# Kernel tuning notes

Hardware: AMD Instinct MI355X
Metric: run time of the kernel (lower is better)

Reference implementation:

```python
import jax, jax.numpy as jnp
import numpy as np

EPS = 1e-8


def setup_inputs() -> dict:
    key = jax.random.key(0)
    ks = jax.random.split(key, 8)
    B, N, D = 8, 1024, 256
    x = jax.random.normal(ks[0], (B, N, D), dtype=jnp.float32)
    y = jax.random.normal(ks[1], (B, N, D), dtype=jnp.float32)
    coords = jax.random.normal(ks[2], (N, N, 6), dtype=jnp.float32)
    # xavier-ish init for U, kaiming-ish for S1/S2
    U = jax.random.normal(ks[3], (D, D), dtype=jnp.float32) * (1.0 / np.sqrt(D))
    S1 = jax.random.normal(ks[4], (D, 1), dtype=jnp.float32)
    S2 = jax.random.normal(ks[5], (D, 1), dtype=jnp.float32)
    gating = jnp.asarray(1.0, dtype=jnp.float32)
    h_temp = jnp.asarray(0.1, dtype=jnp.float32)
    p_temp = jnp.asarray(1.0, dtype=jnp.float32)
    # trunc_normal_(a=0, b=1): std-normal truncated to [0, 1]
    pos_emb = jax.random.truncated_normal(ks[6], 0.0, 1.0, (N, 6, 1)).astype(jnp.float32)
    return {"x": x, "y": y, "coords": coords, "U": U, "S1": S1, "S2": S2,
            "gating": gating, "h_temp": h_temp, "p_temp": p_temp, "pos_emb": pos_emb}


def _spectral(x, U, S):
    # x @ U.T @ diag(|S|) @ U  ==  ((x @ U.T) * |S|) @ U
    s = jnp.abs(S[:, 0])
    return ((x @ U.T) * s) @ U


def reference(x, y, coords, U, S1, S2, gating, h_temp, p_temp, pos_emb):
    B, N, D = x.shape
    scale = D ** (-0.5)
    xs = jnp.stack([_spectral(x, U, S1), _spectral(x, U, S2)], axis=1)  # [B,2,N,D]
    # patch attention scores: [B,2,N,N]
    patch_score = jax.nn.softmax(jnp.einsum('bknd,bmd->bknm', xs, y) * scale, axis=-1)
    # positional scores, shared across batch and the 2 spectral branches: [N,N]
    pos_logits = -jnp.abs(p_temp) * jnp.einsum('nmc,ncq->nm', coords, pos_emb)
    pos_score = jax.nn.softmax(pos_logits, axis=-1)
    g = jax.nn.sigmoid(gating)
    attn = (1.0 - g) * patch_score + g * pos_score[None, None]  # [B,2,N,N]
    # entropy over key axis -> [B,N,2]
    entropy = jnp.sum(-attn * jnp.log(attn + EPS), axis=-1).transpose(0, 2, 1)
    hmap = 2.0 - 2.0 * jax.nn.sigmoid(h_temp * entropy)  # [B,N,2]
    fgbg = hmap[..., 0] >= hmap[..., 1]
    route = jax.lax.stop_gradient(
        jnp.stack([fgbg, ~fgbg], axis=-1).astype(hmap.dtype))  # [B,N,2]
    heat_map = jnp.sum(hmap * route, axis=-1, keepdims=True)  # [B,N,1]
    attn_sel = jnp.sum(attn * route.transpose(0, 2, 1)[..., None], axis=1)  # [B,N,N]
    out = attn_sel @ y  # [B,N,D]
    return (out, heat_map)
```

## Files before the change

kernel.cpp:

```cpp
#include <hip/hip_runtime.h>
#include <hip/hip_bf16.h>
#include <stdint.h>


#define NB 8
#define NN_ 1024
#define ND 256

typedef __bf16 bf16x8 __attribute__((ext_vector_type(8)));
typedef __bf16 bf16x4 __attribute__((ext_vector_type(4)));
typedef float f32x4 __attribute__((ext_vector_type(4)));

__device__ inline void gl_lds(const __bf16* g, __bf16* l) {
    auto gp = (const __attribute__((address_space(1))) uint32_t*)(uintptr_t)g;
    auto lp = (__attribute__((address_space(3))) uint32_t*)(uintptr_t)l;
    __builtin_amdgcn_global_load_lds(gp, lp, 16, 0, 0);
}

__device__ inline float wred_sum(float v) {
#pragma unroll
    for (int o = 32; o; o >>= 1) v += __shfl_xor(v, o, 64);
    return v;
}
__device__ inline float wred_max(float v) {
#pragma unroll
    for (int o = 32; o; o >>= 1) v = fmaxf(v, __shfl_xor(v, o, 64));
    return v;
}

__global__ __launch_bounds__(256) void prep_kernel(
    const float* __restrict__ coords, const float* __restrict__ pos_emb,
    const float* __restrict__ p_temp, const float* __restrict__ x,
    const float* __restrict__ y, const float* __restrict__ U,
    const float* __restrict__ S1, const float* __restrict__ S2,
    float* __restrict__ posS, __bf16* __restrict__ Xh, __bf16* __restrict__ Xl,
    __bf16* __restrict__ yt, __bf16* __restrict__ Yh, __bf16* __restrict__ Yl,
    __bf16* __restrict__ Mh, __bf16* __restrict__ Ml) {
    __shared__ char sm[9216 + 64];
    const int bid = blockIdx.x;
    const int tid = threadIdx.x;

    if (bid < 1024) {
        float* red = (float*)sm;
        const int n = bid;
        const float pt = -fabsf(p_temp[0]);
        float pe[6];
#pragma unroll
        for (int c = 0; c < 6; ++c) pe[c] = pos_emb[n * 6 + c];
        const float* cr = coords + (long)n * NN_ * 6;
        float l[4];
#pragma unroll
        for (int j = 0; j < 4; ++j) {
            const int m = j * 256 + tid;
            const float2* cp = (const float2*)(cr + (long)m * 6);
            float2 c0 = cp[0], c1 = cp[1], c2 = cp[2];
            l[j] = pt * (c0.x * pe[0] + c0.y * pe[1] + c1.x * pe[2] +
                         c1.y * pe[3] + c2.x * pe[4] + c2.y * pe[5]);
        }
        float mx = fmaxf(fmaxf(l[0], l[1]), fmaxf(l[2], l[3]));
        mx = wred_max(mx);
        __syncthreads();
        if ((tid & 63) == 0) red[tid >> 6] = mx;
        __syncthreads();
        mx = fmaxf(fmaxf(red[0], red[1]), fmaxf(red[2], red[3]));
        float e[4], s = 0.f;
#pragma unroll
        for (int j = 0; j < 4; ++j) { e[j] = __expf(l[j] - mx); s += e[j]; }
        s = wred_sum(s);
        __syncthreads();
        if ((tid & 63) == 0) red[4 + (tid >> 6)] = s;
        __syncthreads();
        s = red[4] + red[5] + red[6] + red[7];
        const float inv = 1.f / s;
#pragma unroll
        for (int j = 0; j < 4; ++j)
            posS[(long)n * NN_ + j * 256 + tid] = e[j] * inv;
    } else if (bid < 1536) {
        const int n4 = NB * NN_ * ND / 4;
        int i = (bid - 1024) * 256 + tid;
        for (; i < n4; i += 512 * 256) {
            float4 v = ((const float4*)x)[i];
            bf16x4 h, l;
            h[0] = (__bf16)v.x; l[0] = (__bf16)(v.x - (float)h[0]);
            h[1] = (__bf16)v.y; l[1] = (__bf16)(v.y - (float)h[1]);
            h[2] = (__bf16)v.z; l[2] = (__bf16)(v.z - (float)h[2]);
            h[3] = (__bf16)v.w; l[3] = (__bf16)(v.w - (float)h[3]);
            ((bf16x4*)Xh)[i] = h;
            ((bf16x4*)Xl)[i] = l;
        }
    } else if (bid < 2048) {
        __bf16 (*t)[72] = (__bf16(*)[72])sm;
        const int rem = bid - 1536;
        const int b = rem >> 6;
        const int m0 = (rem & 15) * 64, d0 = ((rem >> 4) & 3) * 64;
        const int c = tid & 15;
        const int r = tid >> 4;
#pragma unroll
        for (int p = 0; p < 4; ++p) {
            const int row = r + p * 16;
            const long gi = ((long)b * NN_ + m0 + row) * ND + d0 + c * 4;
            float4 v = *(const float4*)(y + gi);
            bf16x4 h, l;
            h[0] = (__bf16)v.x; l[0] = (__bf16)(v.x - (float)h[0]);
            h[1] = (__bf16)v.y; l[1] = (__bf16)(v.y - (float)h[1]);
            h[2] = (__bf16)v.z; l[2] = (__bf16)(v.z - (float)h[2]);
            h[3] = (__bf16)v.w; l[3] = (__bf16)(v.w - (float)h[3]);
            *(bf16x4*)(Yh + gi) = h;
            *(bf16x4*)(Yl + gi) = l;
            t[c * 4 + 0][row] = h[0]; t[c * 4 + 1][row] = h[1];
            t[c * 4 + 2][row] = h[2]; t[c * 4 + 3][row] = h[3];
        }
        __syncthreads();
#pragma unroll
        for (int p = 0; p < 4; ++p) {
            const int d = r + p * 16;
            bf16x4 o;
            o[0] = t[d][c * 4 + 0]; o[1] = t[d][c * 4 + 1];
            o[2] = t[d][c * 4 + 2]; o[3] = t[d][c * 4 + 3];
            *(bf16x4*)(yt + ((long)b * ND + d0 + d) * NN_ + m0 + c * 4) = o;
        }
    } else {
        const int n = bid - 2048, j = tid;
        float a1 = 0.f, a2 = 0.f;
        for (int c = 0; c < ND; ++c) {
            const float un = U[c * ND + n];
            const float uj = U[c * ND + j];
            a1 = fmaf(fabsf(S1[c]) * un, uj, a1);
            a2 = fmaf(fabsf(S2[c]) * un, uj, a2);
        }
        const __bf16 h1 = (__bf16)a1, h2 = (__bf16)a2;
        Mh[n * ND + j] = h1;           Ml[n * ND + j] = (__bf16)(a1 - (float)h1);
        Mh[65536 + n * ND + j] = h2;   Ml[65536 + n * ND + j] = (__bf16)(a2 - (float)h2);
    }
}

__global__ __launch_bounds__(256) void mgemm_xs(
    const __bf16* __restrict__ Ah, const __bf16* __restrict__ Al,
    const __bf16* __restrict__ Bh, const __bf16* __restrict__ Bl,
    __bf16* __restrict__ Ch, __bf16* __restrict__ Cl,
    int M, int N, int K, long sB1, long sC) {
    constexpr int BM = 64, BK = 32, BN = 64;
    __shared__ __bf16 As[2][2 * BM * BK];
    __shared__ __bf16 Bs[2][2 * BN * BK];

    const int z = blockIdx.z;
    Bh += (long)z * sB1; Bl += (long)z * sB1;

    const int tid = threadIdx.x;
    const int bm = blockIdx.y * BM, bn = blockIdx.x * BN;
    const int wave = tid >> 6, lane = tid & 63;
    const int wm = wave >> 1, wn = wave & 1;
    const int quad = lane >> 4, l16 = lane & 15;
    const int srow = lane >> 2, slot = lane & 3;

    f32x4 acc[2][2];
#pragma unroll
    for (int i = 0; i < 2; ++i)
#pragma unroll
        for (int j = 0; j < 2; ++j) acc[i][j] = (f32x4){0.f, 0.f, 0.f, 0.f};

    auto stage = [&](int sel, int k0) {
        const int r0 = wave * 16;
        const int row = r0 + srow;
        const int chunk = slot ^ ((row >> 1) & 3);
        const long ga = (long)(bm + row) * K + k0 + chunk * 8;
        gl_lds(Ah + ga, &As[sel][r0 * 32]);
        gl_lds(Al + ga, &As[sel][BM * BK + r0 * 32]);
        const long gb = (long)(bn + row) * K + k0 + chunk * 8;
        gl_lds(Bh + gb, &Bs[sel][r0 * 32]);
        gl_lds(Bl + gb, &Bs[sel][BN * BK + r0 * 32]);
    };

    stage(0, 0);
    __syncthreads();
    int cur = 0;
    for (int k0 = 0; k0 < K; k0 += BK) {
        if (k0 + BK < K) stage(cur ^ 1, k0 + BK);

        bf16x8 a_h[2], a_l[2], b_h[2], b_l[2];
#pragma unroll
        for (int mi = 0; mi < 2; ++mi) {
            const int row = wm * 32 + mi * 16 + l16;
            const int off = row * 32 + ((quad ^ ((row >> 1) & 3)) * 8);
            a_h[mi] = *(const bf16x8*)&As[cur][off];
            a_l[mi] = *(const bf16x8*)&As[cur][BM * BK + off];
        }
#pragma unroll
        for (int ni = 0; ni < 2; ++ni) {
            const int row = wn * 32 + ni * 16 + l16;
            const int off = row * 32 + ((quad ^ ((row >> 1) & 3)) * 8);
            b_h[ni] = *(const bf16x8*)&Bs[cur][off];
            b_l[ni] = *(const bf16x8*)&Bs[cur][BN * BK + off];
        }
#pragma unroll
        for (int mi = 0; mi < 2; ++mi)
#pragma unroll
            for (int ni = 0; ni < 2; ++ni) {
                acc[mi][ni] = __builtin_amdgcn_mfma_f32_16x16x32_bf16(
                    a_h[mi], b_h[ni], acc[mi][ni], 0, 0, 0);
                acc[mi][ni] = __builtin_amdgcn_mfma_f32_16x16x32_bf16(
                    a_h[mi], b_l[ni], acc[mi][ni], 0, 0, 0);
                acc[mi][ni] = __builtin_amdgcn_mfma_f32_16x16x32_bf16(
                    a_l[mi], b_h[ni], acc[mi][ni], 0, 0, 0);
            }

        __syncthreads();
        cur ^= 1;
    }

    Ch += (long)z * sC; Cl += (long)z * sC;
#pragma unroll
    for (int mi = 0; mi < 2; ++mi) {
        const int row0 = bm + wm * 32 + mi * 16 + quad * 4;
#pragma unroll
        for (int ni = 0; ni < 2; ++ni) {
            const int col = bn + wn * 32 + ni * 16 + l16;
#pragma unroll
            for (int r = 0; r < 4; ++r) {
                const float v = acc[mi][ni][r];
                const long idx = (long)(row0 + r) * N + col;
                const __bf16 h = (__bf16)v;
                Ch[idx] = h;
                Cl[idx] = (__bf16)(v - (float)h);
            }
        }
    }
}

__global__ __launch_bounds__(256) void mgemm_sc(
    const __bf16* __restrict__ Ah, const __bf16* __restrict__ Al,
    const __bf16* __restrict__ Bh, const __bf16* __restrict__ Bl,
    float* __restrict__ C, int N, int K,
    long sA1, long sA2, long sB1, long sC, float alpha) {
    constexpr int BM = 128, BK = 32, BN = 128;
    __shared__ __bf16 As[2 * BM * BK];
    __shared__ __bf16 Bs[2 * BN * BK];

    const int bid = blockIdx.x;
    const int xcd = bid & 7;
    const int j   = bid >> 3;
    const int z   = 2 * xcd + (j >> 6);
    const int t   = j & 63;
    const int bm  = (t >> 3) * BM;
    const int bn  = (t & 7) * BN;

    const long aoff = (long)(z >> 1) * sA1 + (long)(z & 1) * sA2;
    const long boff = (long)(z >> 1) * sB1;
    Ah += aoff; Al += aoff;
    Bh += boff; Bl += boff;

    const int tid = threadIdx.x;
    const int wave = tid >> 6, lane = tid & 63;
    const int wm = wave >> 1, wn = wave & 1;
    const int quad = lane >> 4, l16 = lane & 15;

    f32x4 acc[4][4];
#pragma unroll
    for (int i = 0; i < 4; ++i)
#pragma unroll
        for (int jj = 0; jj < 4; ++jj) acc[i][jj] = (f32x4){0.f, 0.f, 0.f, 0.f};

    const int srow = lane >> 2;
    const int slot = lane & 3;

    for (int k0 = 0; k0 < K; k0 += BK) {
        __syncthreads();
#pragma unroll
        for (int i = 0; i < 2; ++i) {
            const int r0 = wave * 32 + i * 16;
            const int row = r0 + srow;
            const int chunk = slot ^ ((row >> 1) & 3);
            const long ga = (long)(bm + row) * K + k0 + chunk * 8;
            gl_lds(Ah + ga, &As[r0 * 32]);
            gl_lds(Al + ga, &As[BM * BK + r0 * 32]);
            const long gb = (long)(bn + row) * K + k0 + chunk * 8;
            gl_lds(Bh + gb, &Bs[r0 * 32]);
            gl_lds(Bl + gb, &Bs[BN * BK + r0 * 32]);
        }
        __syncthreads();

        bf16x8 a_h[4], a_l[4], b_h[4], b_l[4];
#pragma unroll
        for (int mi = 0; mi < 4; ++mi) {
            const int row = wm * 64 + mi * 16 + l16;
            const int off = row * 32 + ((quad ^ ((row >> 1) & 3)) * 8);
            a_h[mi] = *(const bf16x8*)&As[off];
            a_l[mi] = *(const bf16x8*)&As[BM * BK + off];
        }
#pragma unroll
        for (int ni = 0; ni < 4; ++ni) {
            const int row = wn * 64 + ni * 16 + l16;
            const int off = row * 32 + ((quad ^ ((row >> 1) & 3)) * 8);
            b_h[ni] = *(const bf16x8*)&Bs[off];
            b_l[ni] = *(const bf16x8*)&Bs[BN * BK + off];
        }
#pragma unroll
        for (int mi = 0; mi < 4; ++mi)
#pragma unroll
            for (int ni = 0; ni < 4; ++ni) {
                acc[mi][ni] = __builtin_amdgcn_mfma_f32_16x16x32_bf16(
                    a_h[mi], b_h[ni], acc[mi][ni], 0, 0, 0);
                acc[mi][ni] = __builtin_amdgcn_mfma_f32_16x16x32_bf16(
                    a_h[mi], b_l[ni], acc[mi][ni], 0, 0, 0);
                acc[mi][ni] = __builtin_amdgcn_mfma_f32_16x16x32_bf16(
                    a_l[mi], b_h[ni], acc[mi][ni], 0, 0, 0);
            }
    }

    C += (long)z * sC;
#pragma unroll
    for (int mi = 0; mi < 4; ++mi) {
        const int row0 = bm + wm * 64 + mi * 16 + quad * 4;
#pragma unroll
        for (int ni = 0; ni < 4; ++ni) {
            const int col = bn + wn * 64 + ni * 16 + l16;
#pragma unroll
            for (int r = 0; r < 4; ++r)
                C[(long)(row0 + r) * NN_ + col] = acc[mi][ni][r] * alpha;
        }
    }
}

__global__ __launch_bounds__(256, 8) void blendsm_kernel(
    const float* __restrict__ S, const float* __restrict__ pos,
    const float* __restrict__ gating, const float* __restrict__ h_temp,
    __bf16* __restrict__ P, float* __restrict__ heat) {
    const int b = blockIdx.x & 7;
    const int n = (blockIdx.x >> 3) * 4 + (threadIdx.x >> 6);
    const int lane = threadIdx.x & 63;

    const float g = 1.f / (1.f + __expf(-gating[0]));
    const float cg = 1.f - g;
    const float ht = h_temp[0];

    const float* r0p = S + ((long)(b * 2 + 0) * NN_ + n) * NN_;
    const float* r1p = S + ((long)(b * 2 + 1) * NN_ + n) * NN_;

    f32x4 a0[4], a1[4];
#pragma unroll
    for (int j = 0; j < 4; ++j) {
        a0[j] = *(const f32x4*)(r0p + j * 256 + lane * 4);
        a1[j] = *(const f32x4*)(r1p + j * 256 + lane * 4);
    }
    float m0 = -3.4e38f, m1 = -3.4e38f;
#pragma unroll
    for (int j = 0; j < 4; ++j) {
        m0 = fmaxf(m0, fmaxf(fmaxf(a0[j][0], a0[j][1]), fmaxf(a0[j][2], a0[j][3])));
        m1 = fmaxf(m1, fmaxf(fmaxf(a1[j][0], a1[j][1]), fmaxf(a1[j][2], a1[j][3])));
    }
    m0 = wred_max(m0); m1 = wred_max(m1);
    float s0 = 0.f, s1 = 0.f;
#pragma unroll
    for (int j = 0; j < 4; ++j) {
        a0[j][0] = __expf(a0[j][0] - m0); a0[j][1] = __expf(a0[j][1] - m0);
        a0[j][2] = __expf(a0[j][2] - m0); a0[j][3] = __expf(a0[j][3] - m0);
        s0 += a0[j][0] + a0[j][1] + a0[j][2] + a0[j][3];
        a1[j][0] = __expf(a1[j][0] - m1); a1[j][1] = __expf(a1[j][1] - m1);
        a1[j][2] = __expf(a1[j][2] - m1); a1[j][3] = __expf(a1[j][3] - m1);
        s1 += a1[j][0] + a1[j][1] + a1[j][2] + a1[j][3];
    }
    s0 = wred_sum(s0); s1 = wred_sum(s1);
    const float i0 = 1.f / s0, i1 = 1.f / s1;
    const float* pr = pos + (long)n * NN_;
    float e0 = 0.f, e1 = 0.f;
#pragma unroll
    for (int j = 0; j < 4; ++j) {
        const f32x4 pv = *(const f32x4*)(pr + j * 256 + lane * 4);
        a0[j][0] = cg * a0[j][0] * i0 + g * pv[0];
        a0[j][1] = cg * a0[j][1] * i0 + g * pv[1];
        a0[j][2] = cg * a0[j][2] * i0 + g * pv[2];
        a0[j][3] = cg * a0[j][3] * i0 + g * pv[3];
        a1[j][0] = cg * a1[j][0] * i1 + g * pv[0];
        a1[j][1] = cg * a1[j][1] * i1 + g * pv[1];
        a1[j][2] = cg * a1[j][2] * i1 + g * pv[2];
        a1[j][3] = cg * a1[j][3] * i1 + g * pv[3];
        e0 -= a0[j][0] * __logf(a0[j][0] + 1e-8f) + a0[j][1] * __logf(a0[j][1] + 1e-8f) +
              a0[j][2] * __logf(a0[j][2] + 1e-8f) + a0[j][3] * __logf(a0[j][3] + 1e-8f);
        e1 -= a1[j][0] * __logf(a1[j][0] + 1e-8f) + a1[j][1] * __logf(a1[j][1] + 1e-8f) +
              a1[j][2] * __logf(a1[j][2] + 1e-8f) + a1[j][3] * __logf(a1[j][3] + 1e-8f);
    }
    e0 = wred_sum(e0); e1 = wred_sum(e1);
    const float hm0 = 2.f - 2.f / (1.f + __expf(-ht * e0));
    const float hm1 = 2.f - 2.f / (1.f + __expf(-ht * e1));
    const bool fg = (hm0 >= hm1);
    if (lane == 0) heat[(long)b * NN_ + n] = fg ? hm0 : hm1;
    __bf16* prow = P + ((long)b * NN_ + n) * NN_;
#pragma unroll
    for (int j = 0; j < 4; ++j) {
        const f32x4 v = fg ? a0[j] : a1[j];
        bf16x4 o;
        o[0] = (__bf16)v[0]; o[1] = (__bf16)v[1];
        o[2] = (__bf16)v[2]; o[3] = (__bf16)v[3];
        *(bf16x4*)(prow + j * 256 + lane * 4) = o;
    }
}

__global__ __launch_bounds__(256) void pv_gemm(
    const __bf16* __restrict__ A, const __bf16* __restrict__ Bm,
    float* __restrict__ C) {
    constexpr int BM = 32, BK = 32, BN = 64;
    __shared__ __bf16 As[2][BM * BK];
    __shared__ __bf16 Bs[2][BN * BK];

    const int bid = blockIdx.x;
    const int b   = bid & 7;
    const int j   = bid >> 3;
    const int bm  = (j >> 2) * BM;
    const int bn  = (j & 3) * BN;

    A  += (long)b * NN_ * NN_;
    Bm += (long)b * ND * NN_;
    C  += (long)b * NN_ * ND;

    const int tid = threadIdx.x;
    const int wave = tid >> 6, lane = tid & 63;
    const int wm = wave >> 1, wn = wave & 1;
    const int quad = lane >> 4, l16 = lane & 15;
    const int srow = lane >> 2, slot = lane & 3;

    f32x4 acc[2];
    acc[0] = (f32x4){0.f, 0.f, 0.f, 0.f};
    acc[1] = (f32x4){0.f, 0.f, 0.f, 0.f};

    auto stage = [&](int sel, int k0) {
        if (wave < 2) {
            const int row = wave * 16 + srow;
            const int chunk = slot ^ ((row >> 1) & 3);
            gl_lds(A + (long)(bm + row) * NN_ + k0 + chunk * 8,
                   &As[sel][wave * 16 * 32]);
        }
        {
            const int row = wave * 16 + srow;
            const int chunk = slot ^ ((row >> 1) & 3);
            gl_lds(Bm + (long)(bn + row) * NN_ + k0 + chunk * 8,
                   &Bs[sel][wave * 16 * 32]);
        }
    };

    stage(0, 0);
    __syncthreads();
    int cur = 0;
    for (int k0 = 0; k0 < NN_; k0 += BK) {
        if (k0 + BK < NN_) stage(cur ^ 1, k0 + BK);

        const int arow = wm * 16 + l16;
        const int aoff = arow * 32 + ((quad ^ ((arow >> 1) & 3)) * 8);
        bf16x8 a = *(const bf16x8*)&As[cur][aoff];
#pragma unroll
        for (int ni = 0; ni < 2; ++ni) {
            const int brow = wn * 32 + ni * 16 + l16;
            const int boff = brow * 32 + ((quad ^ ((brow >> 1) & 3)) * 8);
            bf16x8 bb = *(const bf16x8*)&Bs[cur][boff];
            acc[ni] = __builtin_amdgcn_mfma_f32_16x16x32_bf16(
                a, bb, acc[ni], 0, 0, 0);
        }

        __syncthreads();
        cur ^= 1;
    }

    const int row0 = bm + wm * 16 + quad * 4;
#pragma unroll
    for (int ni = 0; ni < 2; ++ni) {
        const int col = bn + wn * 32 + ni * 16 + l16;
#pragma unroll
        for (int r = 0; r < 4; ++r)
            C[(long)(row0 + r) * ND + col] = acc[ni][r];
    }
}

extern "C" void kernel_launch(void* const* d_in, const int* in_sizes, int n_in,
                              void* d_out, int out_size, void* d_ws, size_t ws_size,
                              hipStream_t stream) {
    const float* x      = (const float*)d_in[0];
    const float* y      = (const float*)d_in[1];
    const float* coords = (const float*)d_in[2];
    const float* U      = (const float*)d_in[3];
    const float* S1p    = (const float*)d_in[4];
    const float* S2p    = (const float*)d_in[5];
    const float* gating = (const float*)d_in[6];
    const float* h_temp = (const float*)d_in[7];
    const float* p_temp = (const float*)d_in[8];
    const float* pos_emb= (const float*)d_in[9];

    float* out  = (float*)d_out;
    float* heat = out + (long)NB * NN_ * ND;

    char* ws = (char*)d_ws;
    const long MB = 1 << 20;
    float*  Sf  = (float*)(ws);
    float*  pos = (float*)(ws + 64 * MB);
    __bf16* Xh  = (__bf16*)(ws + 68 * MB);
    __bf16* Xl  = (__bf16*)(ws + 72 * MB);
    __bf16* XSh = (__bf16*)(ws + 76 * MB);
    __bf16* XSl = (__bf16*)(ws + 84 * MB);
    __bf16* yt  = (__bf16*)(ws + 92 * MB);
    __bf16* Yh  = (__bf16*)(ws + 96 * MB);
    __bf16* Yl  = (__bf16*)(ws + 100 * MB);
    __bf16* Mh  = (__bf16*)(ws + 104 * MB);
    __bf16* Ml  = Mh + 2 * 65536;
    __bf16* Pb  = (__bf16*)(ws + 76 * MB);

    const long ND2 = (long)NN_ * ND;
    const long BND = (long)NB * ND2;

    prep_kernel<<<dim3(2304), 256, 0, stream>>>(
        coords, pos_emb, p_temp, x, y, U, S1p, S2p,
        pos, Xh, Xl, yt, Yh, Yl, Mh, Ml);

    mgemm_xs<<<dim3(4, 128, 2), 256, 0, stream>>>(
        Xh, Xl, Mh, Ml, XSh, XSl, NB * NN_, ND, ND, 65536, BND);

    mgemm_sc<<<dim3(1024), 256, 0, stream>>>(
        XSh, XSl, Yh, Yl, Sf, NN_, ND,
        ND2, BND, ND2, (long)NN_ * NN_, 0.0625f);

    blendsm_kernel<<<dim3(2048), 256, 0, stream>>>(
        Sf, pos, gating, h_temp, Pb, heat);

    pv_gemm<<<dim3(1024), 256, 0, stream>>>(Pb, yt, out);

    (void)in_sizes; (void)n_in; (void)out_size; (void)ws_size;
}
```

Measured before the change: 196.4 us.

## Rebalance prep work and fuse independent prep tasks into the XS GEMM launch

Splits the prep kernel so only the x split and the M=U^T|S|U build run first. The y conversion/transpose and the positional softmax are folded into the XS GEMM launch as extra blocks, so that independent work fills the GPU alongside the GEMM tiles. The grid layout changes from 3D to a flat 2560 blocks with explicit index decoding, and the M loop is unrolled by 4. This trades a shorter critical path for larger shared memory in the fused kernel and mixed block types within one launch.

Measured after the change: 209.8 us. 1.07x slower.

```diff
diff --git a/kernel.cpp b/kernel.cpp
--- a/kernel.cpp
+++ b/kernel.cpp
@@ -28,56 +28,17 @@
     return v;
 }
 
-__global__ __launch_bounds__(256) void prep_kernel(
-    const float* __restrict__ coords, const float* __restrict__ pos_emb,
-    const float* __restrict__ p_temp, const float* __restrict__ x,
-    const float* __restrict__ y, const float* __restrict__ U,
+__global__ __launch_bounds__(256) void prep1_kernel(
+    const float* __restrict__ x, const float* __restrict__ U,
     const float* __restrict__ S1, const float* __restrict__ S2,
-    float* __restrict__ posS, __bf16* __restrict__ Xh, __bf16* __restrict__ Xl,
-    __bf16* __restrict__ yt, __bf16* __restrict__ Yh, __bf16* __restrict__ Yl,
+    __bf16* __restrict__ Xh, __bf16* __restrict__ Xl,
     __bf16* __restrict__ Mh, __bf16* __restrict__ Ml) {
-    __shared__ char sm[9216 + 64];
     const int bid = blockIdx.x;
     const int tid = threadIdx.x;
 
-    if (bid < 1024) {
-        float* red = (float*)sm;
-        const int n = bid;
-        const float pt = -fabsf(p_temp[0]);
-        float pe[6];
-#pragma unroll
-        for (int c = 0; c < 6; ++c) pe[c] = pos_emb[n * 6 + c];
-        const float* cr = coords + (long)n * NN_ * 6;
-        float l[4];
-#pragma unroll
-        for (int j = 0; j < 4; ++j) {
-            const int m = j * 256 + tid;
-            const float2* cp = (const float2*)(cr + (long)m * 6);
-            float2 c0 = cp[0], c1 = cp[1], c2 = cp[2];
-            l[j] = pt * (c0.x * pe[0] + c0.y * pe[1] + c1.x * pe[2] +
-                         c1.y * pe[3] + c2.x * pe[4] + c2.y * pe[5]);
-        }
-        float mx = fmaxf(fmaxf(l[0], l[1]), fmaxf(l[2], l[3]));
-        mx = wred_max(mx);
-        __syncthreads();
-        if ((tid & 63) == 0) red[tid >> 6] = mx;
-        __syncthreads();
-        mx = fmaxf(fmaxf(red[0], red[1]), fmaxf(red[2], red[3]));
-        float e[4], s = 0.f;
-#pragma unroll
-        for (int j = 0; j < 4; ++j) { e[j] = __expf(l[j] - mx); s += e[j]; }
-        s = wred_sum(s);
-        __syncthreads();
-        if ((tid & 63) == 0) red[4 + (tid >> 6)] = s;
-        __syncthreads();
-        s = red[4] + red[5] + red[6] + red[7];
-        const float inv = 1.f / s;
-#pragma unroll
-        for (int j = 0; j < 4; ++j)
-            posS[(long)n * NN_ + j * 256 + tid] = e[j] * inv;
-    } else if (bid < 1536) {
+    if (bid < 512) {
         const int n4 = NB * NN_ * ND / 4;
-        int i = (bid - 1024) * 256 + tid;
+        int i = bid * 256 + tid;
         for (; i < n4; i += 512 * 256) {
             float4 v = ((const float4*)x)[i];
             bf16x4 h, l;
@@ -88,9 +49,125 @@
             ((bf16x4*)Xh)[i] = h;
             ((bf16x4*)Xl)[i] = l;
         }
-    } else if (bid < 2048) {
-        __bf16 (*t)[72] = (__bf16(*)[72])sm;
-        const int rem = bid - 1536;
+    } else {
+        const int n = bid - 512, j = tid;
+        float a1 = 0.f, a2 = 0.f;
+#pragma unroll 4
+        for (int c = 0; c < ND; ++c) {
+            const float un = U[c * ND + n];
+            const float uj = U[c * ND + j];
+            a1 = fmaf(fabsf(S1[c]) * un, uj, a1);
+            a2 = fmaf(fabsf(S2[c]) * un, uj, a2);
+        }
+        const __bf16 h1 = (__bf16)a1, h2 = (__bf16)a2;
+        Mh[n * ND + j] = h1;           Ml[n * ND + j] = (__bf16)(a1 - (float)h1);
+        Mh[65536 + n * ND + j] = h2;   Ml[65536 + n * ND + j] = (__bf16)(a2 - (float)h2);
+    }
+}
+
+__global__ __launch_bounds__(256) void xs_fused(
+    const __bf16* __restrict__ Ah, const __bf16* __restrict__ Al,
+    const __bf16* __restrict__ Bh, const __bf16* __restrict__ Bl,
+    __bf16* __restrict__ Ch, __bf16* __restrict__ Cl,
+    const float* __restrict__ y, __bf16* __restrict__ yt,
+    __bf16* __restrict__ Yh, __bf16* __restrict__ Yl,
+    const float* __restrict__ coords, const float* __restrict__ pos_emb,
+    const float* __restrict__ p_temp, float* __restrict__ posS) {
+    __shared__ __bf16 sm2[2][8192];
+    const int bid = blockIdx.x;
+    const int tid = threadIdx.x;
+
+    if (bid < 1024) {
+        constexpr int BM = 64, BK = 32, BN = 64;
+        constexpr int K = 256, N = 256;
+        const int z = bid >> 9;
+        const int r = bid & 511;
+        const int bm = (r >> 2) * BM;
+        const int bn = (r & 3) * BN;
+        const __bf16* Bh_ = Bh + (long)z * 65536;
+        const __bf16* Bl_ = Bl + (long)z * 65536;
+
+        const int wave = tid >> 6, lane = tid & 63;
+        const int wm = wave >> 1, wn = wave & 1;
+        const int quad = lane >> 4, l16 = lane & 15;
+        const int srow = lane >> 2, slot = lane & 3;
+
+        f32x4 acc[2][2];
+#pragma unroll
+        for (int i = 0; i < 2; ++i)
+#pragma unroll
+            for (int j = 0; j < 2; ++j) acc[i][j] = (f32x4){0.f, 0.f, 0.f, 0.f};
+
+        auto stage = [&](int sel, int k0) {
+            const int r0 = wave * 16;
+            const int row = r0 + srow;
+            const int chunk = slot ^ ((row >> 1) & 3);
+            const long ga = (long)(bm + row) * K + k0 + chunk * 8;
+            gl_lds(Ah + ga, &sm2[sel][r0 * 32]);
+            gl_lds(Al + ga, &sm2[sel][BM * BK + r0 * 32]);
+            const long gb = (long)(bn + row) * K + k0 + chunk * 8;
+            gl_lds(Bh_ + gb, &sm2[sel][4096 + r0 * 32]);
+            gl_lds(Bl_ + gb, &sm2[sel][4096 + BN * BK + r0 * 32]);
+        };
+
+        stage(0, 0);
+        __syncthreads();
+        int cur = 0;
+        for (int k0 = 0; k0 < K; k0 += BK) {
+            if (k0 + BK < K) stage(cur ^ 1, k0 + BK);
+
+            bf16x8 a_h[2], a_l[2], b_h[2], b_l[2];
+#pragma unroll
+            for (int mi = 0; mi < 2; ++mi) {
+                const int row = wm * 32 + mi * 16 + l16;
+                const int off = row * 32 + ((quad ^ ((row >> 1) & 3)) * 8);
+                a_h[mi] = *(const bf16x8*)&sm2[cur][off];
+                a_l[mi] = *(const bf16x8*)&sm2[cur][BM * BK + off];
+            }
+#pragma unroll
+            for (int ni = 0; ni < 2; ++ni) {
+                const int row = wn * 32 + ni * 16 + l16;
+                const int off = row * 32 + ((quad ^ ((row >> 1) & 3)) * 8);
+                b_h[ni] = *(const bf16x8*)&sm2[cur][4096 + off];
+                b_l[ni] = *(const bf16x8*)&sm2[cur][4096 + BN * BK + off];
+            }
+#pragma unroll
+            for (int mi = 0; mi < 2; ++mi)
+#pragma unroll
+                for (int ni = 0; ni < 2; ++ni) {
+                    acc[mi][ni] = __builtin_amdgcn_mfma_f32_16x16x32_bf16(
+                        a_h[mi], b_h[ni], acc[mi][ni], 0, 0, 0);
+                    acc[mi][ni] = __builtin_amdgcn_mfma_f32_16x16x32_bf16(
+                        a_h[mi], b_l[ni], acc[mi][ni], 0, 0, 0);
+                    acc[mi][ni] = __builtin_amdgcn_mfma_f32_16x16x32_bf16(
+                        a_l[mi], b_h[ni], acc[mi][ni], 0, 0, 0);
+                }
+
+            __syncthreads();
+            cur ^= 1;
+        }
+
+        __bf16* Ch_ = Ch + (long)z * (NB * NN_ * ND);
+        __bf16* Cl_ = Cl + (long)z * (NB * NN_ * ND);
+#pragma unroll
+        for (int mi = 0; mi < 2; ++mi) {
+            const int row0 = bm + wm * 32 + mi * 16 + quad * 4;
+#pragma unroll
+            for (int ni = 0; ni < 2; ++ni) {
+                const int col = bn + wn * 32 + ni * 16 + l16;
+#pragma unroll
+                for (int r2 = 0; r2 < 4; ++r2) {
+                    const float v = acc[mi][ni][r2];
+                    const long idx = (long)(row0 + r2) * N + col;
+                    const __bf16 h = (__bf16)v;
+                    Ch_[idx] = h;
+                    Cl_[idx] = (__bf16)(v - (float)h);
+                }
+            }
+        }
+    } else if (bid < 1536) {
+        __bf16 (*t)[72] = (__bf16(*)[72])&sm2[0][0];
+        const int rem = bid - 1024;
         const int b = rem >> 6;
         const int m0 = (rem & 15) * 64, d0 = ((rem >> 4) & 3) * 64;
         const int c = tid & 15;
@@ -120,110 +197,40 @@
             *(bf16x4*)(yt + ((long)b * ND + d0 + d) * NN_ + m0 + c * 4) = o;
         }
     } else {
-        const int n = bid - 2048, j = tid;
-        float a1 = 0.f, a2 = 0.f;
-        for (int c = 0; c < ND; ++c) {
-            const float un = U[c * ND + n];
-            const float uj = U[c * ND + j];
-            a1 = fmaf(fabsf(S1[c]) * un, uj, a1);
-            a2 = fmaf(fabsf(S2[c]) * un, uj, a2);
-        }
-        const __bf16 h1 = (__bf16)a1, h2 = (__bf16)a2;
-        Mh[n * ND + j] = h1;           Ml[n * ND + j] = (__bf16)(a1 - (float)h1);
-        Mh[65536 + n * ND + j] = h2;   Ml[65536 + n * ND + j] = (__bf16)(a2 - (float)h2);
-    }
-}
-
-__global__ __launch_bounds__(256) void mgemm_xs(
-    const __bf16* __restrict__ Ah, const __bf16* __restrict__ Al,
-    const __bf16* __restrict__ Bh, const __bf16* __restrict__ Bl,
-    __bf16* __restrict__ Ch, __bf16* __restrict__ Cl,
-    int M, int N, int K, long sB1, long sC) {
-    constexpr int BM = 64, BK = 32, BN = 64;
-    __shared__ __bf16 As[2][2 * BM * BK];
-    __shared__ __bf16 Bs[2][2 * BN * BK];
-
-    const int z = blockIdx.z;
-    Bh += (long)z * sB1; Bl += (long)z * sB1;
-
-    const int tid = threadIdx.x;
-    const int bm = blockIdx.y * BM, bn = blockIdx.x * BN;
-    const int wave = tid >> 6, lane = tid & 63;
-    const int wm = wave >> 1, wn = wave & 1;
-    const int quad = lane >> 4, l16 = lane & 15;
-    const int srow = lane >> 2, slot = lane & 3;
-
-    f32x4 acc[2][2];
-#pragma unroll
-    for (int i = 0; i < 2; ++i)
-#pragma unroll
-        for (int j = 0; j < 2; ++j) acc[i][j] = (f32x4){0.f, 0.f, 0.f, 0.f};
-
-    auto stage = [&](int sel, int k0) {
-        const int r0 = wave * 16;
-        const int row = r0 + srow;
-        const int chunk = slot ^ ((row >> 1) & 3);
-        const long ga = (long)(bm + row) * K + k0 + chunk * 8;
-        gl_lds(Ah + ga, &As[sel][r0 * 32]);
-        gl_lds(Al + ga, &As[sel][BM * BK + r0 * 32]);
-        const long gb = (long)(bn + row) * K + k0 + chunk * 8;
-        gl_lds(Bh + gb, &Bs[sel][r0 * 32]);
-        gl_lds(Bl + gb, &Bs[sel][BN * BK + r0 * 32]);
-    };
-
-    stage(0, 0);
-    __syncthreads();
-    int cur = 0;
-    for (int k0 = 0; k0 < K; k0 += BK) {
-        if (k0 + BK < K) stage(cur ^ 1, k0 + BK);
-
-        bf16x8 a_h[2], a_l[2], b_h[2], b_l[2];
-#pragma unroll
-        for (int mi = 0; mi < 2; ++mi) {
-            const int row = wm * 32 + mi * 16 + l16;
-            const int off = row * 32 + ((quad ^ ((row >> 1) & 3)) * 8);
-            a_h[mi] = *(const bf16x8*)&As[cur][off];
-            a_l[mi] = *(const bf16x8*)&As[cur][BM * BK + off];
-        }
-#pragma unroll
-        for (int ni = 0; ni < 2; ++ni) {
-            const int row = wn * 32 + ni * 16 + l16;
-            const int off = row * 32 + ((quad ^ ((row >> 1) & 3)) * 8);
-            b_h[ni] = *(const bf16x8*)&Bs[cur][off];
-            b_l[ni] = *(const bf16x8*)&Bs[cur][BN * BK + off];
-        }
-#pragma unroll
-        for (int mi = 0; mi < 2; ++mi)
-#pragma unroll
-            for (int ni = 0; ni < 2; ++ni) {
-                acc[mi][ni] = __builtin_amdgcn_mfma_f32_16x16x32_bf16(
-                    a_h[mi], b_h[ni], acc[mi][ni], 0, 0, 0);
-                acc[mi][ni] = __builtin_amdgcn_mfma_f32_16x16x32_bf16(
-                    a_h[mi], b_l[ni], acc[mi][ni], 0, 0, 0);
-                acc[mi][ni] = __builtin_amdgcn_mfma_f32_16x16x32_bf16(
-                    a_l[mi], b_h[ni], acc[mi][ni], 0, 0, 0);
-            }
-
-        __syncthreads();
-        cur ^= 1;
-    }
-
-    Ch += (long)z * sC; Cl += (long)z * sC;
-#pragma unroll
-    for (int mi = 0; mi < 2; ++mi) {
-        const int row0 = bm + wm * 32 + mi * 16 + quad * 4;
-#pragma unroll
-        for (int ni = 0; ni < 2; ++ni) {
-            const int col = bn + wn * 32 + ni * 16 + l16;
-#pragma unroll
-            for (int r = 0; r < 4; ++r) {
-                const float v = acc[mi][ni][r];
-                const long idx = (long)(row0 + r) * N + col;
-                const __bf16 h = (__bf16)v;
-                Ch[idx] = h;
-                Cl[idx] = (__bf16)(v - (float)h);
-            }
-        }
+        float* red = (float*)&sm2[0][0];
+        const int n = bid - 1536;
+        const float pt = -fabsf(p_temp[0]);
+        float pe[6];
+#pragma unroll
+        for (int c = 0; c < 6; ++c) pe[c] = pos_emb[n * 6 + c];
+        const float* cr = coords + (long)n * NN_ * 6;
+        float l[4];
+#pragma unroll
+        for (int j = 0; j < 4; ++j) {
+            const int m = j * 256 + tid;
+            const float2* cp = (const float2*)(cr + (long)m * 6);
+            float2 c0 = cp[0], c1 = cp[1], c2 = cp[2];
+            l[j] = pt * (c0.x * pe[0] + c0.y * pe[1] + c1.x * pe[2] +
+                         c1.y * pe[3] + c2.x * pe[4] + c2.y * pe[5]);
+        }
+        float mx = fmaxf(fmaxf(l[0], l[1]), fmaxf(l[2], l[3]));
+        mx = wred_max(mx);
+        __syncthreads();
+        if ((tid & 63) == 0) red[tid >> 6] = mx;
+        __syncthreads();
+        mx = fmaxf(fmaxf(red[0], red[1]), fmaxf(red[2], red[3]));
+        float e[4], s = 0.f;
+#pragma unroll
+        for (int j = 0; j < 4; ++j) { e[j] = __expf(l[j] - mx); s += e[j]; }
+        s = wred_sum(s);
+        __syncthreads();
+        if ((tid & 63) == 0) red[4 + (tid >> 6)] = s;
+        __syncthreads();
+        s = red[4] + red[5] + red[6] + red[7];
+        const float inv = 1.f / s;
+#pragma unroll
+        for (int j = 0; j < 4; ++j)
+            posS[(long)n * NN_ + j * 256 + tid] = e[j] * inv;
     }
 }
 
@@ -504,12 +511,12 @@
     const long ND2 = (long)NN_ * ND;
     const long BND = (long)NB * ND2;
 
-    prep_kernel<<<dim3(2304), 256, 0, stream>>>(
-        coords, pos_emb, p_temp, x, y, U, S1p, S2p,
-        pos, Xh, Xl, yt, Yh, Yl, Mh, Ml);
-
-    mgemm_xs<<<dim3(4, 128, 2), 256, 0, stream>>>(
-        Xh, Xl, Mh, Ml, XSh, XSl, NB * NN_, ND, ND, 65536, BND);
+    prep1_kernel<<<dim3(768), 256, 0, stream>>>(
+        x, U, S1p, S2p, Xh, Xl, Mh, Ml);
+
+    xs_fused<<<dim3(2560), 256, 0, stream>>>(
+        Xh, Xl, Mh, Ml, XSh, XSl,
+        y, yt, Yh, Yl, coords, pos_emb, p_temp, pos);
 
     mgemm_sc<<<dim3(1024), 256, 0, stream>>>(
         XSh, XSl, Yh, Yl, Sf, NN_, ND,
```
